# Performance work log

Hardware: AMD Instinct MI355X
Metric: run time of the kernel (lower is better)

The kernel has to match this reference:

```python
import jax, jax.numpy as jnp
import numpy as np

B, P, T, K = 8, 64, 63, 2        # scenes, proposals/scene, text tokens, target proposals/scene
D, DFF, L = 512, 2048, 2         # d_model, ffn dim, encoder layers
V, NC = 30522, 18                # vocab, classes
DPT, DWD = 1536, 768             # point feats, word feats
S = P + T


def _ln(x, g, b):
    m = x.mean(-1, keepdims=True)
    v = ((x - m) ** 2).mean(-1, keepdims=True)
    return (x - m) * jax.lax.rsqrt(v + 1e-5) * g + b


def _encode(x, mask, enc):
    # post-norm TransformerEncoderLayer (torch default), dropout=0 (eval)
    (qkv_w, qkv_b, out_w, out_b, ln1_g, ln1_b,
     ff1_w, ff1_b, ff2_w, ff2_b, ln2_g, ln2_b) = enc
    for l in range(L):
        qkv = x @ qkv_w[l] + qkv_b[l]
        q, k, v = jnp.split(qkv, 3, axis=-1)
        s = q @ k.T * (1.0 / np.sqrt(D)) + mask
        a = jax.nn.softmax(s, axis=-1) @ v
        x = _ln(x + a @ out_w[l] + out_b[l], ln1_g[l], ln1_b[l])
        f = jax.nn.relu(x @ ff1_w[l] + ff1_b[l]) @ ff2_w[l] + ff2_b[l]
        x = _ln(x + f, ln2_g[l], ln2_b[l])
    return x


def _seq2seq_mask():
    # boxes attend to boxes only; text attends to all boxes + causal text
    i = jnp.arange(S)[:, None]
    j = jnp.arange(S)[None, :]
    allowed = (j < P) | ((i >= P) & (j <= i))
    return jnp.where(allowed, 0.0, -1e9).astype(jnp.float32)


def setup_inputs():
    ks = iter(jax.random.split(jax.random.key(0), 48))

    def nrm(shape, s=0.02):
        return jax.random.normal(next(ks), shape, jnp.float32) * s

    return dict(
        instances=jax.random.normal(next(ks), (B * P, DPT), jnp.float32),
        text_embeddings=jax.random.normal(next(ks), (B, T, DWD), jnp.float32),
        target_proposals=jax.random.randint(next(ks), (B, K), 0, P),
        target_word_ids=jax.random.randint(next(ks), (B, T + 1), 0, V),
        target_classes=jax.random.randint(next(ks), (B,), 0, NC),
        Wi1=nrm((DPT, 1024)), bi1=jnp.zeros((1024,)),
        Wi2=nrm((1024, D)), bi2=jnp.zeros((D,)),
        Ww=nrm((DWD, D)), bw=jnp.zeros((D,)),
        qkv_w=nrm((L, D, 3 * D)), qkv_b=jnp.zeros((L, 3 * D)),
        out_w=nrm((L, D, D)), out_b=jnp.zeros((L, D)),
        ln1_g=jnp.ones((L, D)), ln1_b=jnp.zeros((L, D)),
        ff1_w=nrm((L, D, DFF)), ff1_b=jnp.zeros((L, DFF)),
        ff2_w=nrm((L, DFF, D)), ff2_b=jnp.zeros((L, D)),
        ln2_g=jnp.ones((L, D)), ln2_b=jnp.zeros((L, D)),
        grd_w1=nrm((D, 256)), grd_b1=jnp.zeros((256,)),
        grd_w2=nrm((256, 1)), grd_b2=jnp.zeros((1,)),
        cls_w1=nrm((D, 256)), cls_b1=jnp.zeros((256,)),
        cls_w2=nrm((256, NC)), cls_b2=jnp.zeros((NC,)),
        cap_w1=nrm((D, DWD)), cap_b1=jnp.zeros((DWD,)),
        cap_w2=nrm((DWD, V)), cap_b2=jnp.zeros((V,)),
    )


def reference(instances, text_embeddings, target_proposals, target_word_ids,
              target_classes, Wi1, bi1, Wi2, bi2, Ww, bw, qkv_w, qkv_b, out_w,
              out_b, ln1_g, ln1_b, ff1_w, ff1_b, ff2_w, ff2_b, ln2_g, ln2_b,
              grd_w1, grd_b1, grd_w2, grd_b2, cls_w1, cls_b1, cls_w2, cls_b2,
              cap_w1, cap_b1, cap_w2, cap_b2):
    enc = (qkv_w, qkv_b, out_w, out_b, ln1_g, ln1_b,
           ff1_w, ff1_b, ff2_w, ff2_b, ln2_g, ln2_b)
    box = ((instances @ Wi1 + bi1) @ Wi2 + bi2).reshape(B, P, D)
    txt = text_embeddings @ Ww + bw                                   # [B,T,D]
    # ---- VG branch (unmasked encoder) ----
    vg = jnp.concatenate([box, txt + box.mean(1, keepdims=True)], axis=1)
    out_vg = jax.vmap(lambda x: _encode(x, 0.0, enc))(vg)             # [B,S,D]
    match_scores = (((out_vg[:, :P] @ grd_w1 + grd_b1) @ grd_w2 + grd_b2)
                    .squeeze(-1))                                     # [B,P]
    cls_scores = (out_vg[:, P] @ cls_w1 + cls_b1) @ cls_w2 + cls_b2   # [B,NC]
    # ---- DC branch (seq2seq mask), vmapped over scenes x target proposals ----
    tgt_box = jnp.take_along_axis(box, target_proposals[:, :, None], axis=1)
    cue = txt[:, None] + tgt_box[:, :, None]                          # [B,K,T,D]
    dc = jnp.concatenate(
        [jnp.broadcast_to(box[:, None], (B, K, P, D)), cue], axis=2)  # [B,K,S,D]
    mask = _seq2seq_mask()
    out_dc = jax.vmap(jax.vmap(lambda x: _encode(x, mask, enc)))(dc)
    dc_scores = (out_dc[:, :, P:] @ cap_w1 + cap_b1) @ cap_w2 + cap_b2  # [B,K,T,V]
    # ---- losses ----
    tgt = jnp.zeros((B, P)).at[jnp.arange(B)[:, None], target_proposals].set(1.0 / K)
    match_loss = (-(tgt * jax.nn.log_softmax(match_scores, -1)).sum(-1)).mean()
    cls_lp = jax.nn.log_softmax(cls_scores, -1)
    cls_loss = -jnp.take_along_axis(cls_lp, target_classes[:, None], 1).mean()
    wid = jnp.broadcast_to(target_word_ids[:, None, 1:T + 1], (B, K, T))
    dc_lp = jnp.take_along_axis(jax.nn.log_softmax(dc_scores, -1),
                                wid[..., None], axis=3)[..., 0]       # [B,K,T]
    dc_loss = (-dc_lp.mean(-1)).sum(-1).mean()   # sum over proposals, mean over scenes
    return (match_scores, match_loss, cls_scores, cls_loss, dc_scores, dc_loss)
```

## Files before the change

kernel.cpp:

```cpp
#include <hip/hip_runtime.h>
#include <hip/hip_bf16.h>


typedef __hip_bfloat16 bf16;
typedef __attribute__((ext_vector_type(8))) __bf16 bf16x8;
typedef __attribute__((ext_vector_type(4))) float floatx4;

#define NB 8
#define NP 64
#define NT 63
#define NK 2
#define ND 512
#define NDFF 2048
#define NV 30522
#define NNC 18
#define NS 127
#define NSEQ 24
#define NROWS (NSEQ*NS)

#define OUT_MS 0
#define OUT_MLOSS 512
#define OUT_CS 513
#define OUT_CLOSS 657
#define OUT_DC 658
#define OUT_DCLOSS 30766834

#define C2M 1008
#define C2N 30522
#define C2K 768
#define C2NT 239
#define C2H  478

__device__ __forceinline__ float bflo(unsigned u){ return __uint_as_float(u << 16); }
__device__ __forceinline__ float bfhi(unsigned u){ return __uint_as_float(u & 0xffff0000u); }

__device__ __forceinline__ void gload16(const void* g, void* l) {
    __builtin_amdgcn_global_load_lds(
        (const __attribute__((address_space(1))) unsigned*)g,
        (__attribute__((address_space(3))) unsigned*)l, 16, 0, 0);
}

__global__ __launch_bounds__(256) void gemm_kernel(
    const bf16* __restrict__ A, const bf16* __restrict__ WT,
    const float* __restrict__ bias, const bf16* __restrict__ resid,
    bf16* __restrict__ C, int M, int N, int K, int relu)
{
    __shared__ bf16 As[64 * 32];
    __shared__ bf16 Bs[64 * 32];
    const int tid = threadIdx.x;
    const int m0 = blockIdx.x * 64;
    const int n0 = blockIdx.y * 64;
    const int lane = tid & 63;
    const int wave = tid >> 6;
    const int wm = (wave >> 1) * 32, wn = (wave & 1) * 32;
    const int quad = lane >> 4, r = lane & 15;
    const int srow = tid >> 2;
    const int sk = (tid & 3) * 8;
    const int ar = min(m0 + srow, M - 1);
    const int br = min(n0 + srow, N - 1);
    bf16* lA = As + tid * 8;
    bf16* lB = Bs + tid * 8;

    floatx4 acc[2][2] = {};

    for (int k0 = 0; k0 < K; k0 += 32) {
        __syncthreads();
        gload16(A  + (size_t)ar * K + k0 + sk, lA);
        gload16(WT + (size_t)br * K + k0 + sk, lB);
        __syncthreads();

        bf16x8 a0 = *(const bf16x8*)(&As[(wm + r)      * 32 + quad * 8]);
        bf16x8 a1 = *(const bf16x8*)(&As[(wm + 16 + r) * 32 + quad * 8]);
        bf16x8 b0 = *(const bf16x8*)(&Bs[(wn + r)      * 32 + quad * 8]);
        bf16x8 b1 = *(const bf16x8*)(&Bs[(wn + 16 + r) * 32 + quad * 8]);
        acc[0][0] = __builtin_amdgcn_mfma_f32_16x16x32_bf16(a0, b0, acc[0][0], 0, 0, 0);
        acc[0][1] = __builtin_amdgcn_mfma_f32_16x16x32_bf16(a0, b1, acc[0][1], 0, 0, 0);
        acc[1][0] = __builtin_amdgcn_mfma_f32_16x16x32_bf16(a1, b0, acc[1][0], 0, 0, 0);
        acc[1][1] = __builtin_amdgcn_mfma_f32_16x16x32_bf16(a1, b1, acc[1][1], 0, 0, 0);
    }

    #pragma unroll
    for (int ti = 0; ti < 2; ++ti)
    #pragma unroll
    for (int tj = 0; tj < 2; ++tj) {
        int col = n0 + wn + tj * 16 + r;
        if (col >= N) continue;
        float bvv = bias ? bias[col] : 0.f;
        #pragma unroll
        for (int rr = 0; rr < 4; ++rr) {
            int row = m0 + wm + ti * 16 + quad * 4 + rr;
            if (row >= M) continue;
            float v = acc[ti][tj][rr] + bvv;
            if (resid) v += (float)resid[(size_t)row * N + col];
            if (relu)  v = v > 0.f ? v : 0.f;
            C[(size_t)row * N + col] = __float2bfloat16(v);
        }
    }
}

__global__ __launch_bounds__(256) void gemm128_kernel(
    const bf16* __restrict__ A, const bf16* __restrict__ WT,
    const float* __restrict__ bias, const bf16* __restrict__ resid,
    bf16* __restrict__ C, int M, int N, int K, int relu)
{
    __shared__ bf16 As[128 * 32];
    __shared__ bf16 Bs[128 * 32];
    const int tid = threadIdx.x;
    const int m0 = blockIdx.x * 128;
    const int n0 = blockIdx.y * 128;
    const int lane = tid & 63, wave = tid >> 6;
    const int quad = lane >> 4, r = lane & 15;
    const int wm = (wave >> 1) * 64, wn = (wave & 1) * 64;
    const int srow0 = wave * 32 + (lane >> 2);
    const int srow1 = srow0 + 16;
    const int sk = (lane & 3) * 8;
    const int ar0 = min(m0 + srow0, M - 1), ar1 = min(m0 + srow1, M - 1);
    const int br0 = min(n0 + srow0, N - 1), br1 = min(n0 + srow1, N - 1);
    bf16* lA = As + srow0 * 32 + sk;
    bf16* lB = Bs + srow0 * 32 + sk;

    floatx4 acc[4][4] = {};

    for (int k0 = 0; k0 < K; k0 += 32) {
        __syncthreads();
        gload16(A  + (size_t)ar0 * K + k0 + sk, lA);
        gload16(A  + (size_t)ar1 * K + k0 + sk, lA + 512);
        gload16(WT + (size_t)br0 * K + k0 + sk, lB);
        gload16(WT + (size_t)br1 * K + k0 + sk, lB + 512);
        __syncthreads();

        bf16x8 a[4], b[4];
        #pragma unroll
        for (int ti = 0; ti < 4; ++ti)
            a[ti] = *(const bf16x8*)(&As[(wm + ti * 16 + r) * 32 + quad * 8]);
        #pragma unroll
        for (int tj = 0; tj < 4; ++tj)
            b[tj] = *(const bf16x8*)(&Bs[(wn + tj * 16 + r) * 32 + quad * 8]);
        #pragma unroll
        for (int ti = 0; ti < 4; ++ti)
            #pragma unroll
            for (int tj = 0; tj < 4; ++tj)
                acc[ti][tj] = __builtin_amdgcn_mfma_f32_16x16x32_bf16(a[ti], b[tj], acc[ti][tj], 0, 0, 0);
    }

    #pragma unroll
    for (int ti = 0; ti < 4; ++ti)
    #pragma unroll
    for (int tj = 0; tj < 4; ++tj) {
        int col = n0 + wn + tj * 16 + r;
        if (col >= N) continue;
        float bvv = bias ? bias[col] : 0.f;
        #pragma unroll
        for (int rr = 0; rr < 4; ++rr) {
            int row = m0 + wm + ti * 16 + quad * 4 + rr;
            if (row >= M) continue;
            float v = acc[ti][tj][rr] + bvv;
            if (resid) v += (float)resid[(size_t)row * N + col];
            if (relu)  v = v > 0.f ? v : 0.f;
            C[(size_t)row * N + col] = __float2bfloat16(v);
        }
    }
}

__global__ __launch_bounds__(256) void gemm_cap2_kernel(
    const bf16* __restrict__ A, const bf16* __restrict__ WT,
    const float* __restrict__ bias, float* __restrict__ Cf,
    float2* __restrict__ part)
{
    __shared__ bf16 As[128 * 32];
    __shared__ bf16 Bs[128 * 32];
    const int id = blockIdx.x;
    const int xcd = id & 7, q = id >> 3;
    const int mt = q & 7, cg = q >> 3;
    const int nt = cg * 8 + xcd;
    if (nt >= C2NT) return;
    const int m0 = mt * 128, n0 = nt * 128;

    const int tid = threadIdx.x;
    const int lane = tid & 63, wave = tid >> 6;
    const int quad = lane >> 4, r = lane & 15;
    const int wm = (wave >> 1) * 64, wn = (wave & 1) * 64;
    const int srow0 = wave * 32 + (lane >> 2);
    const int srow1 = srow0 + 16;
    const int sk = (lane & 3) * 8;
    const int ar0 = min(m0 + srow0, C2M - 1), ar1 = min(m0 + srow1, C2M - 1);
    const int br0 = min(n0 + srow0, C2N - 1), br1 = min(n0 + srow1, C2N - 1);
    bf16* lA = As + srow0 * 32 + sk;
    bf16* lB = Bs + srow0 * 32 + sk;

    floatx4 acc[4][4] = {};

    for (int k0 = 0; k0 < C2K; k0 += 32) {
        __syncthreads();
        gload16(A  + (size_t)ar0 * C2K + k0 + sk, lA);
        gload16(A  + (size_t)ar1 * C2K + k0 + sk, lA + 512);
        gload16(WT + (size_t)br0 * C2K + k0 + sk, lB);
        gload16(WT + (size_t)br1 * C2K + k0 + sk, lB + 512);
        __syncthreads();

        bf16x8 a[4], b[4];
        #pragma unroll
        for (int ti = 0; ti < 4; ++ti)
            a[ti] = *(const bf16x8*)(&As[(wm + ti * 16 + r) * 32 + quad * 8]);
        #pragma unroll
        for (int tj = 0; tj < 4; ++tj)
            b[tj] = *(const bf16x8*)(&Bs[(wn + tj * 16 + r) * 32 + quad * 8]);
        #pragma unroll
        for (int ti = 0; ti < 4; ++ti)
            #pragma unroll
            for (int tj = 0; tj < 4; ++tj)
                acc[ti][tj] = __builtin_amdgcn_mfma_f32_16x16x32_bf16(a[ti], b[tj], acc[ti][tj], 0, 0, 0);
    }

    float bv[4];
    bool cok[4];
    #pragma unroll
    for (int tj = 0; tj < 4; ++tj) {
        int col = n0 + wn + tj * 16 + r;
        cok[tj] = (col < C2N);
        bv[tj] = cok[tj] ? bias[col] : 0.f;
    }
    const int half = (wn >> 6);

    #pragma unroll
    for (int ti = 0; ti < 4; ++ti) {
        #pragma unroll
        for (int rr = 0; rr < 4; ++rr) {
            const int rowg = m0 + wm + ti * 16 + quad * 4 + rr;
            const bool rok = (rowg < C2M);
            float v[4], vp[4];
            #pragma unroll
            for (int tj = 0; tj < 4; ++tj) {
                v[tj]  = acc[ti][tj][rr] + bv[tj];
                vp[tj] = cok[tj] ? v[tj] : -1e30f;
            }
            if (rok) {
                float* orow = Cf + (size_t)rowg * C2N;
                #pragma unroll
                for (int tj = 0; tj < 4; ++tj)
                    if (cok[tj]) orow[n0 + wn + tj * 16 + r] = v[tj];
            }
            float mx = fmaxf(fmaxf(vp[0], vp[1]), fmaxf(vp[2], vp[3]));
            #pragma unroll
            for (int o = 1; o < 16; o <<= 1) mx = fmaxf(mx, __shfl_xor(mx, o));
            float s = 0.f;
            #pragma unroll
            for (int tj = 0; tj < 4; ++tj)
                if (cok[tj]) s += __expf(v[tj] - mx);
            #pragma unroll
            for (int o = 1; o < 16; o <<= 1) s += __shfl_xor(s, o);
            if (r == 0 && rok)
                part[(size_t)rowg * C2H + nt * 2 + half] = make_float2(mx, s);
        }
    }
}

struct PrepDesc { const float* src; bf16* dst; int K, N, tx, start, kind; };
struct PrepArgs { PrepDesc d[14]; };

__global__ __launch_bounds__(256) void prep_kernel(PrepArgs pa)
{
    const int bid = blockIdx.x;
    int op = 0;
    #pragma unroll
    for (int i = 1; i < 14; ++i) if (bid >= pa.d[i].start) op = i;
    const PrepDesc D = pa.d[op];
    const int lt = bid - D.start;
    const int tid = threadIdx.x;
    if (D.kind == 1) {
        int base = lt * 1024 + tid * 4;
        float4 v = *(const float4*)(D.src + base);
        bf16 o[4] = { __float2bfloat16(v.x), __float2bfloat16(v.y),
                      __float2bfloat16(v.z), __float2bfloat16(v.w) };
        *(uint2*)(D.dst + base) = *(uint2*)o;
    } else {
        __shared__ float tile[32][33];
        const int tx = tid & 31, ty = tid >> 5;
        const int n0 = (lt % D.tx) * 32, k0 = (lt / D.tx) * 32;
        #pragma unroll
        for (int yy = 0; yy < 32; yy += 8)
            tile[ty + yy][tx] = D.src[(size_t)(k0 + ty + yy) * D.N + n0 + tx];
        __syncthreads();
        #pragma unroll
        for (int yy = 0; yy < 32; yy += 8)
            D.dst[(size_t)(n0 + ty + yy) * D.K + k0 + tx] =
                __float2bfloat16(tile[tx][ty + yy]);
    }
}

__global__ __launch_bounds__(256) void transpose_kernel(
    const float* __restrict__ src, bf16* __restrict__ dst, int K, int N)
{
    __shared__ float tile[32][33];
    const int tx = threadIdx.x & 31, ty = threadIdx.x >> 5;
    const int n0 = blockIdx.x * 32, k0 = blockIdx.y * 32;
    #pragma unroll
    for (int yy = 0; yy < 32; yy += 8) {
        int k = k0 + ty + yy, n = n0 + tx;
        if (k < K && n < N) tile[ty + yy][tx] = src[(size_t)k * N + n];
    }
    __syncthreads();
    #pragma unroll
    for (int yy = 0; yy < 32; yy += 8) {
        int n = n0 + ty + yy, k = k0 + tx;
        if (n < N && k < K) dst[(size_t)n * K + k] = __float2bfloat16(tile[tx][ty + yy]);
    }
}

__global__ __launch_bounds__(256) void box_mean_kernel(
    const bf16* __restrict__ box, float* __restrict__ bm)
{
    const int b = blockIdx.x, tid = threadIdx.x;
    float s0 = 0.f, s1 = 0.f;
    for (int p = 0; p < NP; ++p) {
        const bf16* rw = box + (size_t)(b * NP + p) * ND;
        s0 += (float)rw[tid];
        s1 += (float)rw[tid + 256];
    }
    bm[b * ND + tid]       = s0 * (1.f / 64.f);
    bm[b * ND + tid + 256] = s1 * (1.f / 64.f);
}

__global__ __launch_bounds__(256) void build_x_kernel(
    const bf16* __restrict__ box, const bf16* __restrict__ txt,
    const float* __restrict__ bm, const int* __restrict__ tp,
    bf16* __restrict__ X)
{
    int idx = blockIdx.x * 256 + threadIdx.x;
    if (idx >= NROWS * ND) return;
    int d = idx & (ND - 1);
    int rs = idx >> 9;
    int row = rs % NS, seq = rs / NS;
    float v;
    if (seq < NB) {
        int b = seq;
        if (row < NP) v = (float)box[(size_t)(b * NP + row) * ND + d];
        else v = (float)txt[(size_t)(b * NT + row - NP) * ND + d] + bm[b * ND + d];
    } else {
        int s2 = seq - NB, b = s2 >> 1, k = s2 & 1;
        if (row < NP) v = (float)box[(size_t)(b * NP + row) * ND + d];
        else v = (float)txt[(size_t)(b * NT + row - NP) * ND + d]
               + (float)box[(size_t)(b * NP + tp[b * NK + k]) * ND + d];
    }
    X[idx] = __float2bfloat16(v);
}

__global__ __launch_bounds__(256) void attn_kernel(
    const bf16* __restrict__ QKV, bf16* __restrict__ Aout)
{
    const int blk = blockIdx.x;
    const int seq = blk / NS, i = blk % NS;
    const int tid = threadIdx.x;
    __shared__ float qs[ND];
    __shared__ float sc[128];
    __shared__ float red[64];

    const bf16* qrow = QKV + (size_t)(seq * NS + i) * 1536;
    qs[tid]       = (float)qrow[tid];
    qs[tid + 256] = (float)qrow[tid + 256];
    __syncthreads();

    int jmax = (seq < NB) ? NS : ((i < NP) ? NP : (i + 1));

    if (tid < NS) {
        const uint4* kp = (const uint4*)(QKV + (size_t)(seq * NS + tid) * 1536 + ND);
        float d = 0.f;
        #pragma unroll 4
        for (int c = 0; c < 64; ++c) {
            uint4 u = kp[c];
            int b0 = c * 8;
            d += qs[b0+0]*bflo(u.x) + qs[b0+1]*bfhi(u.x)
               + qs[b0+2]*bflo(u.y) + qs[b0+3]*bfhi(u.y)
               + qs[b0+4]*bflo(u.z) + qs[b0+5]*bfhi(u.z)
               + qs[b0+6]*bflo(u.w) + qs[b0+7]*bfhi(u.w);
        }
        sc[tid] = (tid < jmax) ? d * 0.04419417382415922f : -1e9f;
    } else if (tid == NS) {
        sc[NS] = -1e9f;
    }
    __syncthreads();

    if (tid < 64) red[tid] = fmaxf(sc[tid], sc[tid + 64]);
    __syncthreads();
    for (int s = 32; s > 0; s >>= 1) {
        if (tid < s) red[tid] = fmaxf(red[tid], red[tid + s]);
        __syncthreads();
    }
    float m = red[0];
    __syncthreads();

    if (tid < 128) sc[tid] = __expf(sc[tid] - m);
    __syncthreads();
    if (tid < 64) red[tid] = sc[tid] + sc[tid + 64];
    __syncthreads();
    for (int s = 32; s > 0; s >>= 1) {
        if (tid < s) red[tid] += red[tid + s];
        __syncthreads();
    }
    float inv = 1.f / red[0];

    const unsigned* vp = (const unsigned*)(QKV + (size_t)(seq * NS) * 1536 + 1024);
    float a0 = 0.f, a1 = 0.f;
    for (int j = 0; j < jmax; ++j) {
        float p = sc[j];
        unsigned u = vp[(size_t)j * 768 + tid];
        a0 += p * bflo(u);
        a1 += p * bfhi(u);
    }
    bf16* orow = Aout + (size_t)(seq * NS + i) * ND;
    orow[2 * tid]     = __float2bfloat16(a0 * inv);
    orow[2 * tid + 1] = __float2bfloat16(a1 * inv);
}

__global__ __launch_bounds__(256) void ln_kernel(
    const bf16* __restrict__ Y, const float* __restrict__ g,
    const float* __restrict__ b, bf16* __restrict__ X)
{
    const int row = blockIdx.x, tid = threadIdx.x;
    const bf16* y = Y + (size_t)row * ND;
    float v0 = (float)y[tid], v1 = (float)y[tid + 256];
    __shared__ float rs[256], rq[256];
    rs[tid] = v0 + v1;
    rq[tid] = v0 * v0 + v1 * v1;
    __syncthreads();
    for (int s = 128; s > 0; s >>= 1) {
        if (tid < s) { rs[tid] += rs[tid + s]; rq[tid] += rq[tid + s]; }
        __syncthreads();
    }
    float mean = rs[0] * (1.f / ND);
    float var = rq[0] * (1.f / ND) - mean * mean;
    float rstd = rsqrtf(var + 1e-5f);
    bf16* x = X + (size_t)row * ND;
    x[tid]       = __float2bfloat16((v0 - mean) * rstd * g[tid] + b[tid]);
    x[tid + 256] = __float2bfloat16((v1 - mean) * rstd * g[tid + 256] + b[tid + 256]);
}

__global__ __launch_bounds__(256) void match_head_kernel(
    const bf16* __restrict__ X, const float* __restrict__ w1, const float* __restrict__ b1,
    const float* __restrict__ w2, const float* __restrict__ b2,
    float* __restrict__ msf, float* __restrict__ out)
{
    const int blk = blockIdx.x;
    const int b = blk >> 6, p = blk & 63;
    const int tid = threadIdx.x;
    const bf16* x = X + (size_t)(b * NS + p) * ND;
    __shared__ float xs[ND];
    __shared__ float red[256];
    xs[tid] = (float)x[tid]; xs[tid + 256] = (float)x[tid + 256];
    __syncthreads();
    float h = b1[tid];
    for (int d = 0; d < ND; ++d) h += xs[d] * w1[d * 256 + tid];
    red[tid] = h * w2[tid];
    __syncthreads();
    for (int s = 128; s > 0; s >>= 1) {
        if (tid < s) red[tid] += red[tid + s];
        __syncthreads();
    }
    if (tid == 0) {
        float scv = red[0] + b2[0];
        msf[blk] = scv;
        out[OUT_MS + blk] = scv;
    }
}

__global__ __launch_bounds__(256) void cls_head_kernel(
    const bf16* __restrict__ X, const float* __restrict__ w1, const float* __restrict__ b1,
    const float* __restrict__ w2, const float* __restrict__ b2,
    float* __restrict__ csf, float* __restrict__ out)
{
    const int b = blockIdx.x, tid = threadIdx.x;
    const bf16* x = X + (size_t)(b * NS + NP) * ND;
    __shared__ float xs[ND];
    __shared__ float hs[256];
    xs[tid] = (float)x[tid]; xs[tid + 256] = (float)x[tid + 256];
    __syncthreads();
    float h = b1[tid];
    for (int d = 0; d < ND; ++d) h += xs[d] * w1[d * 256 + tid];
    hs[tid] = h;
    __syncthreads();
    if (tid < NNC) {
        float scv = b2[tid];
        for (int c = 0; c < 256; ++c) scv += hs[c] * w2[c * NNC + tid];
        csf[b * NNC + tid] = scv;
        out[OUT_CS + b * NNC + tid] = scv;
    }
}

__global__ void small_loss_kernel(
    const float* __restrict__ msf, const float* __restrict__ csf,
    const int* __restrict__ tp, const int* __restrict__ tc, float* __restrict__ out)
{
    const int tid = threadIdx.x;
    float mloss = 0.f;
    for (int b = 0; b < NB; ++b) {
        float s = msf[b * NP + tid];
        float m = s;
        for (int o = 32; o > 0; o >>= 1) m = fmaxf(m, __shfl_xor(m, o));
        float e = __expf(s - m);
        float sum = e;
        for (int o = 32; o > 0; o >>= 1) sum += __shfl_xor(sum, o);
        float lse = m + __logf(sum);
        float w = (tid == tp[2 * b] || tid == tp[2 * b + 1]) ? 0.5f : 0.f;
        float c = w * (lse - s);
        for (int o = 32; o > 0; o >>= 1) c += __shfl_xor(c, o);
        mloss += c;
    }
    float closs = 0.f;
    for (int b = 0; b < NB; ++b) {
        float s = (tid < NNC) ? csf[b * NNC + tid] : -1e30f;
        float m = s;
        for (int o = 32; o > 0; o >>= 1) m = fmaxf(m, __shfl_xor(m, o));
        float e = (tid < NNC) ? __expf(s - m) : 0.f;
        float sum = e;
        for (int o = 32; o > 0; o >>= 1) sum += __shfl_xor(sum, o);
        if (tid == 0) closs += (m + __logf(sum)) - csf[b * NNC + tc[b]];
    }
    if (tid == 0) {
        out[OUT_MLOSS] = mloss * (1.f / NB);
        out[OUT_CLOSS] = closs * (1.f / NB);
    }
}

__global__ __launch_bounds__(256) void gather_xc_kernel(
    const bf16* __restrict__ X, bf16* __restrict__ Xc)
{
    int idx = blockIdx.x * 256 + threadIdx.x;
    if (idx >= 1008 * ND) return;
    int d = idx & (ND - 1);
    int r = idx >> 9;
    int seq = NB + r / NT, t = r % NT;
    Xc[idx] = X[(size_t)(seq * NS + NP + t) * ND + d];
}

__global__ void dc_combine_kernel(
    const float2* __restrict__ part, const float* __restrict__ scores,
    const int* __restrict__ twid, float* __restrict__ accf)
{
    const int rr = blockIdx.x, t = threadIdx.x;
    const float2* pr = part + (size_t)rr * C2H;
    float mx = -1e30f;
    for (int i = t; i < C2H; i += 64) mx = fmaxf(mx, pr[i].x);
    for (int o = 1; o < 64; o <<= 1) mx = fmaxf(mx, __shfl_xor(mx, o));
    float s = 0.f;
    for (int i = t; i < C2H; i += 64) {
        float2 p = pr[i];
        s += p.y * __expf(p.x - mx);
    }
    for (int o = 1; o < 64; o <<= 1) s += __shfl_xor(s, o);
    if (t == 0) {
        int b = rr / 126, rem = rr % 126, tok = rem % 63;
        int wid = twid[b * 64 + 1 + tok];
        float lse = mx + __logf(s);
        atomicAdd(accf, (lse - scores[(size_t)rr * C2N + wid]) * (1.f / 504.f));
    }
}

__global__ void init_kernel(float* __restrict__ acc)
{
    if (threadIdx.x < 16) acc[threadIdx.x] = 0.f;
}

__global__ void finalize_kernel(const float* __restrict__ acc, float* __restrict__ out)
{
    out[OUT_DCLOSS] = acc[0];
}

extern "C" void kernel_launch(void* const* d_in, const int* in_sizes, int n_in,
                              void* d_out, int out_size, void* d_ws, size_t ws_size,
                              hipStream_t stream)
{
    const float* instances = (const float*)d_in[0];
    const float* text_emb  = (const float*)d_in[1];
    const int*   tp        = (const int*)d_in[2];
    const int*   twid      = (const int*)d_in[3];
    const int*   tcls      = (const int*)d_in[4];
    const float* Wi1 = (const float*)d_in[5];  const float* bi1 = (const float*)d_in[6];
    const float* Wi2 = (const float*)d_in[7];  const float* bi2 = (const float*)d_in[8];
    const float* Ww  = (const float*)d_in[9];  const float* bw  = (const float*)d_in[10];
    const float* qkv_w = (const float*)d_in[11]; const float* qkv_b = (const float*)d_in[12];
    const float* out_w = (const float*)d_in[13]; const float* out_b = (const float*)d_in[14];
    const float* ln1_g = (const float*)d_in[15]; const float* ln1_b = (const float*)d_in[16];
    const float* ff1_w = (const float*)d_in[17]; const float* ff1_b = (const float*)d_in[18];
    const float* ff2_w = (const float*)d_in[19]; const float* ff2_b = (const float*)d_in[20];
    const float* ln2_g = (const float*)d_in[21]; const float* ln2_b = (const float*)d_in[22];
    const float* grd_w1 = (const float*)d_in[23]; const float* grd_b1 = (const float*)d_in[24];
    const float* grd_w2 = (const float*)d_in[25]; const float* grd_b2 = (const float*)d_in[26];
    const float* cls_w1 = (const float*)d_in[27]; const float* cls_b1 = (const float*)d_in[28];
    const float* cls_w2 = (const float*)d_in[29]; const float* cls_b2 = (const float*)d_in[30];
    const float* cap_w1 = (const float*)d_in[31]; const float* cap_b1 = (const float*)d_in[32];
    const float* cap_w2 = (const float*)d_in[33]; const float* cap_b2 = (const float*)d_in[34];

    float* out = (float*)d_out;

    char* base = (char*)d_ws;
    size_t o = 0;
    auto nxtb = [&](size_t bytes) -> char* {
        char* p = base + o; o += (bytes + 255) & ~(size_t)255; return p;
    };
    float*  bm   = (float*)nxtb(NB * ND * 4);
    float*  msf  = (float*)nxtb(512 * 4);
    float*  csf  = (float*)nxtb(144 * 4);
    float*  accf = (float*)nxtb(64);
    float2* part = (float2*)nxtb((size_t)C2M * C2H * 8);
    bf16* wt_cap1 = (bf16*)nxtb((size_t)768 * 512 * 2);
    bf16* Xc    = (bf16*)nxtb((size_t)1008 * 512 * 2);
    bf16* C1    = (bf16*)nxtb((size_t)1008 * 768 * 2);
    size_t arena0 = o;
    bf16* wt_wi1  = (bf16*)nxtb((size_t)1024 * 1536 * 2);
    bf16* wt_wi2  = (bf16*)nxtb((size_t)512 * 1024 * 2);
    bf16* wt_ww   = (bf16*)nxtb((size_t)512 * 768 * 2);
    bf16* wt_qkv  = (bf16*)nxtb((size_t)2 * 1536 * 512 * 2);
    bf16* wt_out  = (bf16*)nxtb((size_t)2 * 512 * 512 * 2);
    bf16* wt_ff1  = (bf16*)nxtb((size_t)2 * 2048 * 512 * 2);
    bf16* wt_ff2  = (bf16*)nxtb((size_t)2 * 512 * 2048 * 2);
    bf16* inst_b  = (bf16*)nxtb((size_t)512 * 1536 * 2);
    bf16* txt_b   = (bf16*)nxtb((size_t)504 * 768 * 2);
    bf16* box_h   = (bf16*)nxtb((size_t)512 * 1024 * 2);
    bf16* box     = (bf16*)nxtb((size_t)512 * 512 * 2);
    bf16* txt     = (bf16*)nxtb((size_t)504 * 512 * 2);
    bf16* X       = (bf16*)nxtb((size_t)NROWS * ND * 2);
    bf16* QKV     = (bf16*)nxtb((size_t)NROWS * 1536 * 2);
    bf16* Aout    = (bf16*)nxtb((size_t)NROWS * ND * 2);
    bf16* Ybuf    = (bf16*)nxtb((size_t)NROWS * ND * 2);
    bf16* Hbuf    = (bf16*)nxtb((size_t)NROWS * NDFF * 2);
    bf16* wt_cap2 = (bf16*)(base + arena0);

    const dim3 tb(256);

    init_kernel<<<1, 64, 0, stream>>>(accf);

    PrepArgs pa;
    int cur = 0, pi = 0;
    auto addT = [&](const float* s, bf16* d, int K, int N) {
        pa.d[pi] = PrepDesc{ s, d, K, N, N / 32, cur, 0 };
        cur += (N / 32) * (K / 32); pi++;
    };
    auto addC = [&](const float* s, bf16* d, int elems) {
        pa.d[pi] = PrepDesc{ s, d, 0, 0, 0, cur, 1 };
        cur += elems / 1024; pi++;
    };
    addT(Wi1, wt_wi1, 1536, 1024);
    addT(Wi2, wt_wi2, 1024, 512);
    addT(Ww,  wt_ww,  768,  512);
    for (int l = 0; l < 2; ++l) {
        addT(qkv_w + (size_t)l * 512 * 1536, wt_qkv + (size_t)l * 1536 * 512, 512, 1536);
        addT(out_w + (size_t)l * 512 * 512,  wt_out + (size_t)l * 512 * 512,  512, 512);
        addT(ff1_w + (size_t)l * 512 * 2048, wt_ff1 + (size_t)l * 2048 * 512, 512, 2048);
        addT(ff2_w + (size_t)l * 2048 * 512, wt_ff2 + (size_t)l * 512 * 2048, 2048, 512);
    }
    addT(cap_w1, wt_cap1, 512, 768);
    addC(instances, inst_b, 512 * 1536);
    addC(text_emb,  txt_b,  504 * 768);
    prep_kernel<<<cur, tb, 0, stream>>>(pa);

    auto G64 = [&](const bf16* A, const bf16* WT, const float* bias, const bf16* resid,
                   bf16* C, int M, int N, int K, int relu) {
        dim3 g((M + 63) / 64, (N + 63) / 64);
        gemm_kernel<<<g, tb, 0, stream>>>(A, WT, bias, resid, C, M, N, K, relu);
    };
    auto G128 = [&](const bf16* A, const bf16* WT, const float* bias, const bf16* resid,
                    bf16* C, int M, int N, int K, int relu) {
        dim3 g((M + 127) / 128, (N + 127) / 128);
        gemm128_kernel<<<g, tb, 0, stream>>>(A, WT, bias, resid, C, M, N, K, relu);
    };

    G64(inst_b, wt_wi1, bi1, nullptr, box_h, 512, 1024, 1536, 0);
    G64(box_h,  wt_wi2, bi2, nullptr, box,   512, 512,  1024, 0);
    G64(txt_b,  wt_ww,  bw,  nullptr, txt,   504, 512,  768,  0);

    box_mean_kernel<<<NB, tb, 0, stream>>>(box, bm);
    build_x_kernel<<<(NROWS * ND) / 256, tb, 0, stream>>>(box, txt, bm, tp, X);

    for (int l = 0; l < 2; ++l) {
        G128(X, wt_qkv + (size_t)l * 1536 * 512, qkv_b + l * 1536, nullptr, QKV,
             NROWS, 1536, 512, 0);
        attn_kernel<<<NROWS, tb, 0, stream>>>(QKV, Aout);
        G64(Aout, wt_out + (size_t)l * 512 * 512, out_b + l * 512, X, Ybuf,
            NROWS, 512, 512, 0);
        ln_kernel<<<NROWS, tb, 0, stream>>>(Ybuf, ln1_g + l * 512, ln1_b + l * 512, X);
        G128(X, wt_ff1 + (size_t)l * 2048 * 512, ff1_b + l * 2048, nullptr, Hbuf,
             NROWS, 2048, 512, 1);
        G64(Hbuf, wt_ff2 + (size_t)l * 512 * 2048, ff2_b + l * 512, X, Ybuf,
            NROWS, 512, 2048, 0);
        ln_kernel<<<NROWS, tb, 0, stream>>>(Ybuf, ln2_g + l * 512, ln2_b + l * 512, X);
    }

    match_head_kernel<<<512, tb, 0, stream>>>(X, grd_w1, grd_b1, grd_w2, grd_b2, msf, out);
    cls_head_kernel<<<NB, tb, 0, stream>>>(X, cls_w1, cls_b1, cls_w2, cls_b2, csf, out);
    small_loss_kernel<<<1, 64, 0, stream>>>(msf, csf, tp, tcls, out);

    gather_xc_kernel<<<(1008 * ND) / 256, tb, 0, stream>>>(X, Xc);
    G64(Xc, wt_cap1, cap_b1, nullptr, C1, 1008, 768, 512, 0);

    {
        dim3 g((C2N + 31) / 32, (C2K + 31) / 32);
        transpose_kernel<<<g, tb, 0, stream>>>(cap_w2, wt_cap2, C2K, C2N);
    }
    gemm_cap2_kernel<<<8 * 8 * 30, tb, 0, stream>>>(C1, wt_cap2, cap_b2,
                                                    out + OUT_DC, part);

    dc_combine_kernel<<<1008, 64, 0, stream>>>(part, out + OUT_DC, twid, accf);
    finalize_kernel<<<1, 1, 0, stream>>>(accf, out);

    (void)in_sizes; (void)n_in; (void)out_size; (void)ws_size;
}
```

Baseline: 898.0 us.

## Double-buffer LDS tiles in vocab projection GEMM to overlap loads with MFMA

```diff
diff --git a/kernel.cpp b/kernel.cpp
--- a/kernel.cpp
+++ b/kernel.cpp
@@ -167,8 +167,8 @@
     const float* __restrict__ bias, float* __restrict__ Cf,
     float2* __restrict__ part)
 {
-    __shared__ bf16 As[128 * 32];
-    __shared__ bf16 Bs[128 * 32];
+    __shared__ bf16 As[2][128 * 32];
+    __shared__ bf16 Bs[2][128 * 32];
     const int id = blockIdx.x;
     const int xcd = id & 7, q = id >> 3;
     const int mt = q & 7, cg = q >> 3;
@@ -181,35 +181,47 @@
     const int quad = lane >> 4, r = lane & 15;
     const int wm = (wave >> 1) * 64, wn = (wave & 1) * 64;
     const int srow0 = wave * 32 + (lane >> 2);
-    const int srow1 = srow0 + 16;
     const int sk = (lane & 3) * 8;
-    const int ar0 = min(m0 + srow0, C2M - 1), ar1 = min(m0 + srow1, C2M - 1);
-    const int br0 = min(n0 + srow0, C2N - 1), br1 = min(n0 + srow1, C2N - 1);
-    bf16* lA = As + srow0 * 32 + sk;
-    bf16* lB = Bs + srow0 * 32 + sk;
+    const int ar0 = min(m0 + srow0,      C2M - 1), ar1 = min(m0 + srow0 + 16, C2M - 1);
+    const int br0 = min(n0 + srow0,      C2N - 1), br1 = min(n0 + srow0 + 16, C2N - 1);
+    const bf16* aR0 = A  + (size_t)ar0 * C2K + sk;
+    const bf16* aR1 = A  + (size_t)ar1 * C2K + sk;
+    const bf16* bR0 = WT + (size_t)br0 * C2K + sk;
+    const bf16* bR1 = WT + (size_t)br1 * C2K + sk;
+    const int soff = srow0 * 32 + sk;
 
     floatx4 acc[4][4] = {};
 
-    for (int k0 = 0; k0 < C2K; k0 += 32) {
-        __syncthreads();
-        gload16(A  + (size_t)ar0 * C2K + k0 + sk, lA);
-        gload16(A  + (size_t)ar1 * C2K + k0 + sk, lA + 512);
-        gload16(WT + (size_t)br0 * C2K + k0 + sk, lB);
-        gload16(WT + (size_t)br1 * C2K + k0 + sk, lB + 512);
-        __syncthreads();
-
+    gload16(aR0, &As[0][soff]);
+    gload16(aR1, &As[0][soff + 512]);
+    gload16(bR0, &Bs[0][soff]);
+    gload16(bR1, &Bs[0][soff + 512]);
+    __syncthreads();
+
+    int cur = 0;
+    #pragma unroll 1
+    for (int t = 0; t < 24; ++t) {
+        if (t + 1 < 24) {
+            const int k1 = (t + 1) * 32;
+            gload16(aR0 + k1, &As[cur ^ 1][soff]);
+            gload16(aR1 + k1, &As[cur ^ 1][soff + 512]);
+            gload16(bR0 + k1, &Bs[cur ^ 1][soff]);
+            gload16(bR1 + k1, &Bs[cur ^ 1][soff + 512]);
+        }
         bf16x8 a[4], b[4];
         #pragma unroll
         for (int ti = 0; ti < 4; ++ti)
-            a[ti] = *(const bf16x8*)(&As[(wm + ti * 16 + r) * 32 + quad * 8]);
+            a[ti] = *(const bf16x8*)(&As[cur][(wm + ti * 16 + r) * 32 + quad * 8]);
         #pragma unroll
         for (int tj = 0; tj < 4; ++tj)
-            b[tj] = *(const bf16x8*)(&Bs[(wn + tj * 16 + r) * 32 + quad * 8]);
+            b[tj] = *(const bf16x8*)(&Bs[cur][(wn + tj * 16 + r) * 32 + quad * 8]);
         #pragma unroll
         for (int ti = 0; ti < 4; ++ti)
             #pragma unroll
             for (int tj = 0; tj < 4; ++tj)
                 acc[ti][tj] = __builtin_amdgcn_mfma_f32_16x16x32_bf16(a[ti], b[tj], acc[ti][tj], 0, 0, 0);
+        __syncthreads();
+        cur ^= 1;
     }
 
     float bv[4];
```

Measured after the change: 898.8 us. About the same (+0.1%).
